# Kernel optimization log

Measured on AMD Instinct MI355X. Metric: run time of the kernel, lower is better.

The kernel has to match this reference:

```python
import jax, jax.numpy as jnp
import numpy as np

N = 10000          # nodes
E = 320000         # edges (avg degree 32)
IN_DIM = 128
H = 4              # num_head_NCLA
C = 64             # num_hidden (per-head out channels of conv1)
NEG_SLOPE = 0.2
BN_EPS = 1e-5


def setup_inputs() -> dict:
    key = jax.random.key(0)
    ks = jax.random.split(key, 8)
    x = jax.random.normal(ks[0], (N, IN_DIM), jnp.float32)
    edge_index = jax.random.randint(ks[1], (2, E), 0, N).astype(jnp.int64)
    # GATConv params: lin (no bias), att_src/att_dst [1,H,C], final bias [H*C]
    W = jax.random.normal(ks[2], (IN_DIM, H * C), jnp.float32) / np.sqrt(IN_DIM).astype(np.float32)
    att_src = jax.random.normal(ks[3], (H, C), jnp.float32) * 0.1
    att_dst = jax.random.normal(ks[4], (H, C), jnp.float32) * 0.1
    bias = jnp.zeros((H * C,), jnp.float32)
    # bn1 affine params (shared across both BN applications, as in source)
    gamma = jnp.ones((H * C,), jnp.float32)
    beta = jnp.zeros((H * C,), jnp.float32)
    return dict(x=x, edge_index=edge_index, W=W, att_src=att_src,
                att_dst=att_dst, bias=bias, gamma=gamma, beta=beta)


def _batchnorm(x, gamma, beta):
    # BatchNorm1d, training-mode stats (batch mean, biased variance)
    mu = jnp.mean(x, axis=0)
    var = jnp.mean(jnp.square(x - mu), axis=0)
    return (x - mu) * jax.lax.rsqrt(var + BN_EPS) * gamma + beta


def _gat_conv(x, edge_index, W, att_src, att_dst, bias):
    src, dst = edge_index[0], edge_index[1]
    xp = (x @ W).reshape(-1, H, C)                      # [N,H,C]
    a_src = jnp.einsum('nhc,hc->nh', xp, att_src)       # [N,H]
    a_dst = jnp.einsum('nhc,hc->nh', xp, att_dst)       # [N,H]
    logits = a_src[src] + a_dst[dst]                    # [E,H]
    logits = jnp.where(logits >= 0, logits, NEG_SLOPE * logits)  # leaky_relu
    # scatter-softmax over incoming edges of each dst node
    m = jax.ops.segment_max(logits, dst, num_segments=N)         # [N,H]
    m = jnp.where(jnp.isfinite(m), m, 0.0)              # empty segments -> 0
    e = jnp.exp(logits - m[dst])                        # [E,H]
    denom = jax.ops.segment_sum(e, dst, num_segments=N)          # [N,H]
    alpha = e / (denom[dst] + 1e-16)                    # [E,H]
    msg = xp[src] * alpha[:, :, None]                   # [E,H,C]
    out = jax.ops.segment_sum(msg, dst, num_segments=N) # [N,H,C]
    return out.reshape(-1, H * C) + bias, alpha


def reference(x, edge_index, W, att_src, att_dst, bias, gamma, beta):
    x1, alpha = _gat_conv(x, edge_index, W, att_src, att_dst, bias)
    x2 = _batchnorm(x1, gamma, beta)
    x_ = _batchnorm(jax.nn.elu(x2), gamma, beta)        # bn1 reused, as in source
    heads = jnp.moveaxis(x_.reshape(-1, H, C), 1, 0)    # [H,N,C]: per-head splits
    return heads, alpha
```

## Files before the change

### kernel.cpp

```cpp
#include <hip/hip_runtime.h>
#include <math.h>

#define INDIM 128
#define HC 256
#define NH 4
#define CAP 128
#define NSHARD 64
#define BROWS 20

typedef unsigned short ushort_t;

__device__ __forceinline__ unsigned int f2bf_u(float f) {
  unsigned int u = __float_as_uint(f);
  return (u + 0x7FFFu + ((u >> 16) & 1u)) >> 16;
}
__device__ __forceinline__ float bf2f(ushort_t u) {
  return __uint_as_float(((unsigned int)u) << 16);
}

__global__ __launch_bounds__(256) void gemm_att_bucket_kernel(
    const float* __restrict__ x, const float* __restrict__ W,
    const float* __restrict__ att_s, const float* __restrict__ att_d,
    const int* __restrict__ dst, int* __restrict__ cnt,
    int* __restrict__ bucket, int E, int epb, ushort_t* __restrict__ xpb,
    float* __restrict__ a_src, float* __restrict__ a_dst, int N) {
  constexpr int RM = 32;
  __shared__ __align__(16) float xs[RM * INDIM];
  int tid = threadIdx.x;
  {
    int e0 = blockIdx.x * epb;
    int e1 = min(e0 + epb, E);
    for (int e = e0 + tid; e < e1; e += 256) {
      int d = dst[e];
      int pos = atomicAdd(&cnt[d], 1);
      if (pos < CAP) bucket[(size_t)d * CAP + pos] = e;
    }
  }
  int n0 = blockIdx.x * RM;
  int nrows = min(RM, N - n0);
  if (nrows <= 0) return;
  if (nrows == RM) {
    const float4* xg = (const float4*)(x + (size_t)n0 * INDIM);
    float4* xs4 = (float4*)xs;
    xs4[tid] = xg[tid];
    xs4[tid + 256] = xg[tid + 256];
    xs4[tid + 512] = xg[tid + 512];
    xs4[tid + 768] = xg[tid + 768];
  } else {
    for (int i = tid; i < RM * INDIM; i += 256) {
      int r = i / INDIM;
      xs[i] = (r < nrows) ? x[(size_t)(n0 + r) * INDIM + (i % INDIM)] : 0.f;
    }
  }
  __syncthreads();

  int lane = tid & 63;
  int wv = tid >> 6;
  int col = lane * 4;
  int row0 = wv * 8;

  float4 acc[8];
#pragma unroll
  for (int r = 0; r < 8; ++r) acc[r] = make_float4(0.f, 0.f, 0.f, 0.f);

  for (int k0 = 0; k0 < INDIM; k0 += 4) {
    float4 w0 = *(const float4*)&W[(size_t)(k0 + 0) * HC + col];
    float4 w1 = *(const float4*)&W[(size_t)(k0 + 1) * HC + col];
    float4 w2 = *(const float4*)&W[(size_t)(k0 + 2) * HC + col];
    float4 w3 = *(const float4*)&W[(size_t)(k0 + 3) * HC + col];
#pragma unroll
    for (int r = 0; r < 8; ++r) {
      float4 xv = *(const float4*)&xs[(row0 + r) * INDIM + k0];
      acc[r].x = fmaf(xv.w, w3.x, fmaf(xv.z, w2.x, fmaf(xv.y, w1.x, fmaf(xv.x, w0.x, acc[r].x))));
      acc[r].y = fmaf(xv.w, w3.y, fmaf(xv.z, w2.y, fmaf(xv.y, w1.y, fmaf(xv.x, w0.y, acc[r].y))));
      acc[r].z = fmaf(xv.w, w3.z, fmaf(xv.z, w2.z, fmaf(xv.y, w1.z, fmaf(xv.x, w0.z, acc[r].z))));
      acc[r].w = fmaf(xv.w, w3.w, fmaf(xv.z, w2.w, fmaf(xv.y, w1.w, fmaf(xv.x, w0.w, acc[r].w))));
    }
  }

  float4 as4 = *(const float4*)&att_s[col];
  float4 ad4 = *(const float4*)&att_d[col];
  int h = lane >> 4;
#pragma unroll
  for (int r = 0; r < 8; ++r) {
    int row = row0 + r;
    if (row >= nrows) break;
    float4 a = acc[r];
    uint2 pk;
    pk.x = f2bf_u(a.x) | (f2bf_u(a.y) << 16);
    pk.y = f2bf_u(a.z) | (f2bf_u(a.w) << 16);
    *(uint2*)&xpb[(size_t)(n0 + row) * HC + col] = pk;
    float ps = a.x * as4.x + a.y * as4.y + a.z * as4.z + a.w * as4.w;
    float pd = a.x * ad4.x + a.y * ad4.y + a.z * ad4.z + a.w * ad4.w;
#pragma unroll
    for (int o = 8; o > 0; o >>= 1) {
      ps += __shfl_xor(ps, o);
      pd += __shfl_xor(pd, o);
    }
    if ((lane & 15) == 0) {
      a_src[(n0 + row) * NH + h] = ps;
      a_dst[(n0 + row) * NH + h] = pd;
    }
  }
}

__global__ __launch_bounds__(256) void node_kernel(
    const int* __restrict__ cnt, const int* __restrict__ bucket,
    const int* __restrict__ src_arr, const float* __restrict__ a_src,
    const float* __restrict__ a_dst, const ushort_t* __restrict__ xpb,
    const float* __restrict__ bias, float* __restrict__ x1,
    float* __restrict__ alpha_out, float* __restrict__ shards, int N) {
  int n = blockIdx.x;
  int tid = threadIdx.x;
  int lane = tid & 63, wv = tid >> 6;
  int deg = min(cnt[n], CAP);
  float bv = bias[tid];
  int shb = (n & (NSHARD - 1)) * (2 * HC);
  if (deg == 0) {
    x1[(size_t)n * HC + tid] = bv;
    atomicAdd(&shards[shb + tid], bv);
    atomicAdd(&shards[shb + HC + tid], bv * bv);
    return;
  }
  const int* brow = bucket + (size_t)n * CAP;

  __shared__ float m_s[NH], d_s[NH];
  __shared__ __align__(16) float alpha_lds[NH * CAP];
  __shared__ __align__(16) int src_lds[CAP];

  {
    int h = wv;
    float adst = a_dst[n * NH + h];
    float m = -INFINITY, s = 0.f;
    for (int i = lane; i < deg; i += 64) {
      int sidx = src_arr[brow[i]];
      if (h == 0) src_lds[i] = sidx;
      float l = a_src[sidx * NH + h] + adst;
      l = (l >= 0.f) ? l : 0.2f * l;
      if (l > m) { s = s * __expf(m - l) + 1.f; m = l; }
      else s += __expf(l - m);
    }
#pragma unroll
    for (int o = 32; o > 0; o >>= 1) {
      float m2 = __shfl_xor(m, o);
      float s2 = __shfl_xor(s, o);
      float M = fmaxf(m, m2);
      float sa = (m > -INFINITY) ? s * __expf(m - M) : 0.f;
      float sb = (m2 > -INFINITY) ? s2 * __expf(m2 - M) : 0.f;
      m = M; s = sa + sb;
    }
    if (lane == 0) { m_s[h] = m; d_s[h] = s + 1e-16f; }
  }
  __syncthreads();

  float m_r[NH], dinv_r[NH], adst_r[NH];
#pragma unroll
  for (int h = 0; h < NH; ++h) {
    m_r[h] = m_s[h];
    dinv_r[h] = 1.0f / d_s[h];
    adst_r[h] = a_dst[n * NH + h];
  }

  int cpad = (deg + 3) & ~3;
  if (tid < deg) {
    int sidx = src_lds[tid];
    float4 as4 = *(const float4*)&a_src[sidx * NH];
    const float* ap = (const float*)&as4;
    float4 av;
    float* avp = (float*)&av;
#pragma unroll
    for (int h = 0; h < NH; ++h) {
      float l = ap[h] + adst_r[h];
      l = (l >= 0.f) ? l : 0.2f * l;
      float a = __expf(l - m_r[h]) * dinv_r[h];
      alpha_lds[h * CAP + tid] = a;
      avp[h] = a;
    }
    *(float4*)&alpha_out[(size_t)brow[tid] * NH] = av;
  } else if (tid < cpad) {
    src_lds[tid] = 0;
#pragma unroll
    for (int h = 0; h < NH; ++h) alpha_lds[h * CAP + tid] = 0.f;
  }
  __syncthreads();

  float acc0 = 0.f, acc1 = 0.f, acc2 = 0.f, acc3 = 0.f;
  int hbase = wv * CAP;
  for (int i = 0; i < cpad; i += 4) {
    float4 a4 = *(const float4*)&alpha_lds[hbase + i];
    int4 s4 = *(const int4*)&src_lds[i];
    ushort_t u0 = xpb[(size_t)s4.x * HC + tid];
    ushort_t u1 = xpb[(size_t)s4.y * HC + tid];
    ushort_t u2 = xpb[(size_t)s4.z * HC + tid];
    ushort_t u3 = xpb[(size_t)s4.w * HC + tid];
    acc0 = fmaf(a4.x, bf2f(u0), acc0);
    acc1 = fmaf(a4.y, bf2f(u1), acc1);
    acc2 = fmaf(a4.z, bf2f(u2), acc2);
    acc3 = fmaf(a4.w, bf2f(u3), acc3);
  }
  float v = (acc0 + acc1) + (acc2 + acc3) + bv;
  x1[(size_t)n * HC + tid] = v;
  atomicAdd(&shards[shb + tid], v);
  atomicAdd(&shards[shb + HC + tid], v * v);
}

__global__ __launch_bounds__(256) void bn_stats2_kernel(
    const float* __restrict__ x1, const float* __restrict__ shards,
    const float* __restrict__ gamma, const float* __restrict__ beta,
    float* __restrict__ sums2, int N) {
  int t = threadIdx.x;
  float s1 = 0.f, q1 = 0.f;
#pragma unroll
  for (int k = 0; k < NSHARD; ++k) {
    s1 += shards[k * (2 * HC) + t];
    q1 += shards[k * (2 * HC) + HC + t];
  }
  float mu = s1 * (1.f / N);
  float var = q1 * (1.f / N) - mu * mu;
  float inv = rsqrtf(var + 1e-5f);
  float g = gamma[t], b = beta[t];
  int r0 = blockIdx.x * BROWS;
  int rend = min(r0 + BROWS, N);
  float s = 0.f, q = 0.f;
  for (int r = r0; r < rend; ++r) {
    float v = x1[(size_t)r * HC + t];
    float x2 = fmaf((v - mu) * inv, g, b);
    float e = x2 > 0.f ? x2 : expm1f(x2);
    s += e; q = fmaf(e, e, q);
  }
  atomicAdd(&sums2[t], s);
  atomicAdd(&sums2[HC + t], q);
}

__global__ __launch_bounds__(256) void bn_final_kernel(
    const float* __restrict__ x1, const float* __restrict__ shards,
    const float* __restrict__ sums2, const float* __restrict__ gamma,
    const float* __restrict__ beta, float* __restrict__ out, int N) {
  int t = threadIdx.x;
  float s1 = 0.f, q1 = 0.f;
#pragma unroll
  for (int k = 0; k < NSHARD; ++k) {
    s1 += shards[k * (2 * HC) + t];
    q1 += shards[k * (2 * HC) + HC + t];
  }
  float mu1 = s1 * (1.f / N);
  float var1 = q1 * (1.f / N) - mu1 * mu1;
  float inv1 = rsqrtf(var1 + 1e-5f);
  float mu2 = sums2[t] * (1.f / N);
  float var2 = sums2[HC + t] * (1.f / N) - mu2 * mu2;
  float inv2 = rsqrtf(var2 + 1e-5f);
  float g = gamma[t], b = beta[t];
  int h = t >> 6, c = t & 63;
  int r0 = blockIdx.x * BROWS;
  int rend = min(r0 + BROWS, N);
  for (int r = r0; r < rend; ++r) {
    float v = x1[(size_t)r * HC + t];
    float x2 = fmaf((v - mu1) * inv1, g, b);
    float e = x2 > 0.f ? x2 : expm1f(x2);
    out[(size_t)h * N * 64 + (size_t)r * 64 + c] = fmaf((e - mu2) * inv2, g, b);
  }
}

extern "C" void kernel_launch(void* const* d_in, const int* in_sizes, int n_in,
                              void* d_out, int out_size, void* d_ws, size_t ws_size,
                              hipStream_t stream) {
  const float* x     = (const float*)d_in[0];
  const int*   edge  = (const int*)d_in[1];
  const float* W     = (const float*)d_in[2];
  const float* att_s = (const float*)d_in[3];
  const float* att_d = (const float*)d_in[4];
  const float* bias  = (const float*)d_in[5];
  const float* gamma = (const float*)d_in[6];
  const float* beta  = (const float*)d_in[7];

  int N = in_sizes[0] / INDIM;
  int E = in_sizes[1] / 2;
  const int* src = edge;
  const int* dst = edge + E;

  char* ws = (char*)d_ws;
  size_t o = 0;
  auto alloc = [&](size_t bytes) {
    void* p = ws + o;
    o += (bytes + 255) & ~(size_t)255;
    return p;
  };
  ushort_t* xpb     = (ushort_t*)alloc((size_t)N * HC * 2);
  float* x1         = (float*)alloc((size_t)N * HC * 4);
  float* a_src      = (float*)alloc((size_t)N * NH * 4);
  float* a_dst      = (float*)alloc((size_t)N * NH * 4);
  char*  zbase      = (char*)alloc(0);
  int*   cnt        = (int*)alloc((size_t)N * 4);
  float* shards     = (float*)alloc((size_t)NSHARD * 2 * HC * 4);
  float* sums2      = (float*)alloc(2 * HC * 4);
  size_t zbytes     = (size_t)((char*)alloc(0) - zbase);
  int*   bucket     = (int*)alloc((size_t)N * CAP * 4);

  float* out_heads = (float*)d_out;
  float* out_alpha = out_heads + (size_t)NH * N * 64;

  hipMemsetAsync(zbase, 0, zbytes, stream);

  int gblocks = (N + 31) / 32;
  int epb = (E + gblocks - 1) / gblocks;
  gemm_att_bucket_kernel<<<gblocks, 256, 0, stream>>>(
      x, W, att_s, att_d, dst, cnt, bucket, E, epb, xpb, a_src, a_dst, N);
  node_kernel<<<N, 256, 0, stream>>>(cnt, bucket, src, a_src, a_dst, xpb, bias,
                                     x1, out_alpha, shards, N);
  int bnb = (N + BROWS - 1) / BROWS;
  bn_stats2_kernel<<<bnb, 256, 0, stream>>>(x1, shards, gamma, beta, sums2, N);
  bn_final_kernel<<<bnb, 256, 0, stream>>>(x1, shards, sums2, gamma, beta,
                                           out_heads, N);
}
```

Before: 114.2 us.

## Stage W through shared memory and halve GEMM row tile per block

The fused GEMM/bucketing kernel now loads W into shared memory in four 32-row chunks and reads it from LDS instead of global memory. The row tile drops from 32 to 16 per block, which doubles the grid, and the edge-bucketing atomics move after the GEMM so they no longer delay it. The intent is more parallelism and less global-load latency on W, at the cost of 32KB extra LDS per block, extra barriers, and W being reloaded by twice as many blocks.

```diff
diff --git a/kernel.cpp b/kernel.cpp
--- a/kernel.cpp
+++ b/kernel.cpp
@@ -24,83 +24,98 @@
     const int* __restrict__ dst, int* __restrict__ cnt,
     int* __restrict__ bucket, int E, int epb, ushort_t* __restrict__ xpb,
     float* __restrict__ a_src, float* __restrict__ a_dst, int N) {
-  constexpr int RM = 32;
+  constexpr int RM = 16;
   __shared__ __align__(16) float xs[RM * INDIM];
+  __shared__ __align__(16) float4 wq[32 * 64];
   int tid = threadIdx.x;
-  {
-    int e0 = blockIdx.x * epb;
-    int e1 = min(e0 + epb, E);
-    for (int e = e0 + tid; e < e1; e += 256) {
-      int d = dst[e];
-      int pos = atomicAdd(&cnt[d], 1);
-      if (pos < CAP) bucket[(size_t)d * CAP + pos] = e;
-    }
-  }
   int n0 = blockIdx.x * RM;
   int nrows = min(RM, N - n0);
-  if (nrows <= 0) return;
-  if (nrows == RM) {
-    const float4* xg = (const float4*)(x + (size_t)n0 * INDIM);
-    float4* xs4 = (float4*)xs;
-    xs4[tid] = xg[tid];
-    xs4[tid + 256] = xg[tid + 256];
-    xs4[tid + 512] = xg[tid + 512];
-    xs4[tid + 768] = xg[tid + 768];
-  } else {
-    for (int i = tid; i < RM * INDIM; i += 256) {
-      int r = i / INDIM;
-      xs[i] = (r < nrows) ? x[(size_t)(n0 + r) * INDIM + (i % INDIM)] : 0.f;
-    }
-  }
-  __syncthreads();
-
-  int lane = tid & 63;
-  int wv = tid >> 6;
-  int col = lane * 4;
-  int row0 = wv * 8;
-
-  float4 acc[8];
-#pragma unroll
-  for (int r = 0; r < 8; ++r) acc[r] = make_float4(0.f, 0.f, 0.f, 0.f);
-
-  for (int k0 = 0; k0 < INDIM; k0 += 4) {
-    float4 w0 = *(const float4*)&W[(size_t)(k0 + 0) * HC + col];
-    float4 w1 = *(const float4*)&W[(size_t)(k0 + 1) * HC + col];
-    float4 w2 = *(const float4*)&W[(size_t)(k0 + 2) * HC + col];
-    float4 w3 = *(const float4*)&W[(size_t)(k0 + 3) * HC + col];
-#pragma unroll
-    for (int r = 0; r < 8; ++r) {
-      float4 xv = *(const float4*)&xs[(row0 + r) * INDIM + k0];
-      acc[r].x = fmaf(xv.w, w3.x, fmaf(xv.z, w2.x, fmaf(xv.y, w1.x, fmaf(xv.x, w0.x, acc[r].x))));
-      acc[r].y = fmaf(xv.w, w3.y, fmaf(xv.z, w2.y, fmaf(xv.y, w1.y, fmaf(xv.x, w0.y, acc[r].y))));
-      acc[r].z = fmaf(xv.w, w3.z, fmaf(xv.z, w2.z, fmaf(xv.y, w1.z, fmaf(xv.x, w0.z, acc[r].z))));
-      acc[r].w = fmaf(xv.w, w3.w, fmaf(xv.z, w2.w, fmaf(xv.y, w1.w, fmaf(xv.x, w0.w, acc[r].w))));
-    }
-  }
-
-  float4 as4 = *(const float4*)&att_s[col];
-  float4 ad4 = *(const float4*)&att_d[col];
-  int h = lane >> 4;
-#pragma unroll
-  for (int r = 0; r < 8; ++r) {
-    int row = row0 + r;
-    if (row >= nrows) break;
-    float4 a = acc[r];
-    uint2 pk;
-    pk.x = f2bf_u(a.x) | (f2bf_u(a.y) << 16);
-    pk.y = f2bf_u(a.z) | (f2bf_u(a.w) << 16);
-    *(uint2*)&xpb[(size_t)(n0 + row) * HC + col] = pk;
-    float ps = a.x * as4.x + a.y * as4.y + a.z * as4.z + a.w * as4.w;
-    float pd = a.x * ad4.x + a.y * ad4.y + a.z * ad4.z + a.w * ad4.w;
-#pragma unroll
-    for (int o = 8; o > 0; o >>= 1) {
-      ps += __shfl_xor(ps, o);
-      pd += __shfl_xor(pd, o);
-    }
-    if ((lane & 15) == 0) {
-      a_src[(n0 + row) * NH + h] = ps;
-      a_dst[(n0 + row) * NH + h] = pd;
-    }
+
+  if (nrows > 0) {
+    if (nrows == RM) {
+      const float4* xg = (const float4*)(x + (size_t)n0 * INDIM);
+      float4* xs4 = (float4*)xs;
+      xs4[tid] = xg[tid];
+      xs4[tid + 256] = xg[tid + 256];
+    } else {
+      for (int i = tid; i < RM * INDIM; i += 256) {
+        int r = i / INDIM;
+        xs[i] = (r < nrows) ? x[(size_t)(n0 + r) * INDIM + (i % INDIM)] : 0.f;
+      }
+    }
+
+    int lane = tid & 63;
+    int wv = tid >> 6;
+    int row0 = wv * 4;
+
+    float4 acc[4];
+#pragma unroll
+    for (int r = 0; r < 4; ++r) acc[r] = make_float4(0.f, 0.f, 0.f, 0.f);
+
+    const float4* W4 = (const float4*)W;
+#pragma unroll 1
+    for (int p = 0; p < 4; ++p) {
+      if (p) __syncthreads();
+      const float4* Wg = W4 + (size_t)p * 2048;
+#pragma unroll
+      for (int j = 0; j < 8; ++j) wq[tid + j * 256] = Wg[tid + j * 256];
+      __syncthreads();
+#pragma unroll 1
+      for (int c = 0; c < 4; ++c) {
+        int kl = c * 8;
+        int kg = p * 32 + kl;
+        float4 w[8];
+#pragma unroll
+        for (int j = 0; j < 8; ++j) w[j] = wq[(kl + j) * 64 + lane];
+#pragma unroll
+        for (int r = 0; r < 4; ++r) {
+          float4 xa = *(const float4*)&xs[(row0 + r) * INDIM + kg];
+          float4 xb = *(const float4*)&xs[(row0 + r) * INDIM + kg + 4];
+          acc[r].x = fmaf(xb.w, w[7].x, fmaf(xb.z, w[6].x, fmaf(xb.y, w[5].x, fmaf(xb.x, w[4].x,
+                     fmaf(xa.w, w[3].x, fmaf(xa.z, w[2].x, fmaf(xa.y, w[1].x, fmaf(xa.x, w[0].x, acc[r].x))))))));
+          acc[r].y = fmaf(xb.w, w[7].y, fmaf(xb.z, w[6].y, fmaf(xb.y, w[5].y, fmaf(xb.x, w[4].y,
+                     fmaf(xa.w, w[3].y, fmaf(xa.z, w[2].y, fmaf(xa.y, w[1].y, fmaf(xa.x, w[0].y, acc[r].y))))))));
+          acc[r].z = fmaf(xb.w, w[7].z, fmaf(xb.z, w[6].z, fmaf(xb.y, w[5].z, fmaf(xb.x, w[4].z,
+                     fmaf(xa.w, w[3].z, fmaf(xa.z, w[2].z, fmaf(xa.y, w[1].z, fmaf(xa.x, w[0].z, acc[r].z))))))));
+          acc[r].w = fmaf(xb.w, w[7].w, fmaf(xb.z, w[6].w, fmaf(xb.y, w[5].w, fmaf(xb.x, w[4].w,
+                     fmaf(xa.w, w[3].w, fmaf(xa.z, w[2].w, fmaf(xa.y, w[1].w, fmaf(xa.x, w[0].w, acc[r].w))))))));
+        }
+      }
+    }
+
+    int col = lane * 4;
+    float4 as4 = *(const float4*)&att_s[col];
+    float4 ad4 = *(const float4*)&att_d[col];
+    int h = lane >> 4;
+#pragma unroll
+    for (int r = 0; r < 4; ++r) {
+      int row = row0 + r;
+      if (row >= nrows) break;
+      float4 a = acc[r];
+      uint2 pk;
+      pk.x = f2bf_u(a.x) | (f2bf_u(a.y) << 16);
+      pk.y = f2bf_u(a.z) | (f2bf_u(a.w) << 16);
+      *(uint2*)&xpb[(size_t)(n0 + row) * HC + col] = pk;
+      float ps = a.x * as4.x + a.y * as4.y + a.z * as4.z + a.w * as4.w;
+      float pd = a.x * ad4.x + a.y * ad4.y + a.z * ad4.z + a.w * ad4.w;
+#pragma unroll
+      for (int o = 8; o > 0; o >>= 1) {
+        ps += __shfl_xor(ps, o);
+        pd += __shfl_xor(pd, o);
+      }
+      if ((lane & 15) == 0) {
+        a_src[(n0 + row) * NH + h] = ps;
+        a_dst[(n0 + row) * NH + h] = pd;
+      }
+    }
+  }
+
+  int e0 = blockIdx.x * epb;
+  int e1 = min(e0 + epb, E);
+  for (int e = e0 + tid; e < e1; e += 256) {
+    int d = dst[e];
+    int pos = atomicAdd(&cnt[d], 1);
+    if (pos < CAP) bucket[(size_t)d * CAP + pos] = e;
   }
 }
 
@@ -301,7 +316,7 @@
 
   hipMemsetAsync(zbase, 0, zbytes, stream);
 
-  int gblocks = (N + 31) / 32;
+  int gblocks = (N + 15) / 16;
   int epb = (E + gblocks - 1) / gblocks;
   gemm_att_bucket_kernel<<<gblocks, 256, 0, stream>>>(
       x, W, att_s, att_d, dst, cnt, bucket, E, epb, xpb, a_src, a_dst, N);
```

New measurement: 105.1 us. -7.9%, faster.
